# Kernel optimization log

Measured on AMD Instinct MI355X. Metric: run time of the kernel, lower is better.

Reference implementation:

```python
import jax, jax.numpy as jnp
import numpy as np

I_T = 0.5       # IoU threshold self.I_t
GAMMA = 2.0     # focal loss gamma
EPS = 1e-7      # focal loss eps clamp
BS, P, C_IN = 8, 2048, 512


def pairwise_iou(b):
    # b: (bs, P, 4) xyxy -> (bs, P, P), same math as torchvision box_iou (no +1)
    area = (b[..., 2] - b[..., 0]) * (b[..., 3] - b[..., 1])
    lt = jnp.maximum(b[:, :, None, :2], b[:, None, :, :2])
    rb = jnp.minimum(b[:, :, None, 2:], b[:, None, :, 2:])
    wh = jnp.clip(rb - lt, 0.0, None)
    inter = wh[..., 0] * wh[..., 1]
    return inter / (area[:, :, None] + area[:, None, :] - inter)


def assign_labels_weights(pre_score, labels, rois):
    # Vectorized, order-faithful version of the per-batch/per-class python loop.
    # Selected seeds per class c: proposals with pre_score[...,c] > 0.5 if more than
    # one, else the single argmax proposal (torch code falls back when k<=1).
    # Sequential `_I > old` running max over (c, j) in ascending order is equivalent
    # to a global first-occurrence argmax (strict >), so per-class max + running
    # compare with earlier-class tie preference reproduces it exactly.
    bs, Pn = pre_score.shape[0], pre_score.shape[1]
    iou = pairwise_iou(rois)                      # (bs, P, P)
    run_I = jnp.full((bs, Pn), -1.0, pre_score.dtype)
    run_w = jnp.ones((bs, Pn), pre_score.dtype)
    hits = []
    for c in range(3):
        s = pre_score[:, :, c]                    # (bs, P)
        th = s > 0.5
        cnt = th.sum(-1)
        onehot = jnp.arange(Pn)[None, :] == jnp.argmax(s, -1)[:, None]
        sel = jnp.where((cnt > 1)[:, None], th, onehot)
        sel = sel & (labels[:, c] != 0)[:, None]  # skip classes absent from image
        masked = jnp.where(sel[:, None, :], iou, -2.0)  # (bs, P, P)
        val = masked.max(-1)                      # best IoU vs any seed of class c
        jidx = masked.argmax(-1)
        cand_x = jnp.take_along_axis(s, jidx, axis=1)
        better = val > run_I
        run_w = jnp.where(better, cand_x, run_w)
        run_I = jnp.where(better, val, run_I)
        hits.append(val > I_T)
    hit = jnp.stack(hits, -1)                     # (bs, P, 3)
    bg = (~hit.any(-1))[..., None]
    y = jnp.concatenate([hit.astype(pre_score.dtype), bg.astype(pre_score.dtype)], -1)
    return y, run_w


def icr_forward(inputs, fc_w, fc_b, pre_score, labels, rois, num):
    bs = inputs.shape[0] // num
    xr = inputs @ fc_w + fc_b                     # (bs*P, 4)
    logit = jax.nn.softmax(xr.reshape(bs, num, 4), -1)
    ps = jax.lax.stop_gradient(pre_score)         # .clone().detach()
    lb = jax.lax.stop_gradient(labels)
    y, w = assign_labels_weights(ps, lb, rois)
    y = y.reshape(bs * num, 4)
    w = w.reshape(bs * num, 1)
    # FocalLoss(gamma=2, mode='none')
    p = jnp.clip(jax.nn.softmax(xr, -1), EPS, 1.0 - EPS)
    fl = -y * jnp.log(p) * (1.0 - p) ** GAMMA
    imbalance = y.sum(0)                          # (4,)
    loss = (w * fl / (imbalance + 1e-7)).reshape(bs, num, 4)
    lab = lb.at[:, 3].set(1.0)[:, None, :]        # lab[:,0,3]=1
    w_ = 10.0 * jnp.exp(logit) * (1.0 - lab) + lab
    loss = (loss * w_).sum() / bs
    return logit, loss


def setup_inputs():
    key = jax.random.key(0)
    k = jax.random.split(key, 6)
    inputs = jax.random.normal(k[0], (BS * P, C_IN), jnp.float32)
    fc_w = jax.random.normal(k[1], (C_IN, 4), jnp.float32) * 0.02
    fc_b = jnp.zeros((4,), jnp.float32)
    pre_score = jax.random.uniform(k[2], (BS, P, 4), dtype=jnp.float32)
    labels = (jax.random.uniform(k[3], (BS, 4)) < 0.5).astype(jnp.float32)
    labels = labels.at[:, 3].set(0.0)
    xy = jax.random.uniform(k[4], (BS, P, 2), dtype=jnp.float32) * 448.0
    wh = jax.random.uniform(k[5], (BS, P, 2), dtype=jnp.float32) * 63.0 + 1.0
    rois = jnp.concatenate([xy, xy + wh], -1)     # valid xyxy boxes in 512x512
    return {"inputs": inputs, "fc_w": fc_w, "fc_b": fc_b, "pre_score": pre_score,
            "labels": labels, "rois": rois, "num": P}


def reference(inputs, fc_w, fc_b, pre_score, labels, rois, num):
    return icr_forward(inputs, fc_w, fc_b, pre_score, labels, rois, num)
```

## Files before the change

### kernel.cpp

```cpp
#include <hip/hip_runtime.h>

#define BSZ 8
#define PN  2048
#define CIN 512
#define CAP 2048
#define NW  16


__global__ __launch_bounds__(256) void k_front(
    const float* __restrict__ inp, const float* __restrict__ fcw,
    const float* __restrict__ fcb, const float* __restrict__ ps,
    const float* __restrict__ labels, const float* __restrict__ rois,
    float* __restrict__ logit, float* __restrict__ accum,
    int* __restrict__ meta, float* __restrict__ sList,
    float* __restrict__ areaL, float4* __restrict__ roiList)
{
  const int t = threadIdx.x;
  if (blockIdx.x < 1024) {
    const int gw   = (blockIdx.x * 256 + t) >> 6;
    const int lane = t & 63;
    const int kb   = lane << 2;
    const float4 wa0 = *(const float4*)(fcw + (kb + 0) * 4);
    const float4 wa1 = *(const float4*)(fcw + (kb + 1) * 4);
    const float4 wa2 = *(const float4*)(fcw + (kb + 2) * 4);
    const float4 wa3 = *(const float4*)(fcw + (kb + 3) * 4);
    const float4 wb0 = *(const float4*)(fcw + (256 + kb + 0) * 4);
    const float4 wb1 = *(const float4*)(fcw + (256 + kb + 1) * 4);
    const float4 wb2 = *(const float4*)(fcw + (256 + kb + 2) * 4);
    const float4 wb3 = *(const float4*)(fcw + (256 + kb + 3) * 4);
    const float4 bias = *(const float4*)fcb;
    #pragma unroll
    for (int rr = 0; rr < 4; ++rr) {
      const int r = (gw << 2) + rr;
      const float* row = inp + r * CIN;
      const float4 xa = *(const float4*)(row + kb);
      const float4 xb = *(const float4*)(row + 256 + kb);
      float a0 = xa.x*wa0.x + xa.y*wa1.x + xa.z*wa2.x + xa.w*wa3.x
               + xb.x*wb0.x + xb.y*wb1.x + xb.z*wb2.x + xb.w*wb3.x;
      float a1 = xa.x*wa0.y + xa.y*wa1.y + xa.z*wa2.y + xa.w*wa3.y
               + xb.x*wb0.y + xb.y*wb1.y + xb.z*wb2.y + xb.w*wb3.y;
      float a2 = xa.x*wa0.z + xa.y*wa1.z + xa.z*wa2.z + xa.w*wa3.z
               + xb.x*wb0.z + xb.y*wb1.z + xb.z*wb2.z + xb.w*wb3.z;
      float a3 = xa.x*wa0.w + xa.y*wa1.w + xa.z*wa2.w + xa.w*wa3.w
               + xb.x*wb0.w + xb.y*wb1.w + xb.z*wb2.w + xb.w*wb3.w;
      #pragma unroll
      for (int off = 32; off; off >>= 1) {
        a0 += __shfl_xor(a0, off); a1 += __shfl_xor(a1, off);
        a2 += __shfl_xor(a2, off); a3 += __shfl_xor(a3, off);
      }
      if (lane == 0) {
        a0 += bias.x; a1 += bias.y; a2 += bias.z; a3 += bias.w;
        const float m  = fmaxf(fmaxf(a0, a1), fmaxf(a2, a3));
        const float e0 = expf(a0 - m), e1 = expf(a1 - m);
        const float e2 = expf(a2 - m), e3 = expf(a3 - m);
        const float inv = 1.0f / (e0 + e1 + e2 + e3);
        float4 o; o.x = e0*inv; o.y = e1*inv; o.z = e2*inv; o.w = e3*inv;
        *(float4*)(logit + r * 4) = o;
      }
    }
    return;
  }

  const int bc = blockIdx.x - 1024;
  if (bc == 0 && t < 8) accum[t] = 0.0f;
  const int b = bc / 3;
  const int c = bc % 3;
  const int j0 = t * 8;

  float sv[8];
  int   flg = 0, cnt = 0;
  float vmax = -1e30f;
  int   jmax = 0;
  #pragma unroll
  for (int m = 0; m < 8; ++m) {
    const float s = ps[(b * PN + j0 + m) * 4 + c];
    sv[m] = s;
    if (s > 0.5f) { flg |= 1 << m; ++cnt; }
    if (s > vmax) { vmax = s; jmax = j0 + m; }
  }

  __shared__ float lv[256];
  __shared__ int   lj[256];
  __shared__ int   pre[256];
  lv[t] = vmax; lj[t] = jmax; pre[t] = cnt;
  __syncthreads();
  for (int off = 128; off > 0; off >>= 1) {
    if (t < off) {
      const float v2 = lv[t + off]; const int j2 = lj[t + off];
      if (v2 > lv[t] || (v2 == lv[t] && j2 < lj[t])) { lv[t] = v2; lj[t] = j2; }
    }
    __syncthreads();
  }
  for (int off = 1; off < 256; off <<= 1) {
    const int add = (t >= off) ? pre[t - off] : 0;
    __syncthreads();
    pre[t] += add;
    __syncthreads();
  }
  const int  totalTh = pre[255];
  const int  excl    = pre[t] - cnt;
  const int  jArg    = lj[0];
  const bool lab     = labels[b * 4 + c] != 0.0f;
  const int  L    = (!lab) ? 0 : ((totalTh > 1) ? totalTh : 1);
  const int  Lpad = (L + 7) & ~7;

  __shared__ float4 lastRoi;
  __shared__ float  lastS, lastA;
  float4* dstR = roiList + bc * CAP;
  float*  dstS = sList   + bc * CAP;
  float*  dstA = areaL   + bc * CAP;
  const float4* rb = ((const float4*)rois) + b * PN;

  if (lab) {
    if (totalTh > 1) {
      int pos = excl;
      #pragma unroll
      for (int m = 0; m < 8; ++m) {
        if (flg & (1 << m)) {
          const float4 r = rb[j0 + m];
          const float  a = (r.z - r.x) * (r.w - r.y);
          dstR[pos] = r; dstS[pos] = sv[m]; dstA[pos] = a;
          if (pos == L - 1) { lastRoi = r; lastS = sv[m]; lastA = a; }
          ++pos;
        }
      }
    } else if (t == (jArg >> 3)) {
      const float4 r = rb[jArg];
      const float  a = (r.z - r.x) * (r.w - r.y);
      dstR[0] = r; dstS[0] = sv[jArg & 7]; dstA[0] = a;
      lastRoi = r; lastS = sv[jArg & 7]; lastA = a;
    }
  }
  __syncthreads();
  if (t < Lpad - L) { dstR[L + t] = lastRoi; dstS[L + t] = lastS; dstA[L + t] = lastA; }
  if (t == 0) meta[bc] = Lpad;
}

__global__ __launch_bounds__(1024, 8) void k_assign(
    const float* __restrict__ rois, const int* __restrict__ meta,
    const float4* __restrict__ roiList, const float* __restrict__ areaL,
    float* __restrict__ pbn, float* __restrict__ pbd, int* __restrict__ pbp)
{
  const int blk   = blockIdx.x;
  const int h     = blk & 1;
  const int itile = (blk >> 1) & 31;
  const int b     = blk >> 6;
  const int t     = threadIdx.x;
  const int lane  = t & 63;
  const int wv    = t >> 6;

  __shared__ __align__(16) char ldsraw[61440];
  float4* sroi  = (float4*)ldsraw;
  float*  sarea = (float*)(ldsraw + 49152);
  float*  mn    = (float*)ldsraw;
  float*  md    = (float*)(ldsraw + 12288);
  int*    mp    = (int*)(ldsraw + 24576);

  int startc[3], cntc[3];
  #pragma unroll
  for (int c = 0; c < 3; ++c) {
    const int L  = meta[b * 3 + c];
    const int L2 = ((L >> 1) + 7) & ~7;
    const int s0 = h ? L2 : 0;
    const int e0 = h ? L  : L2;
    startc[c] = s0;
    cntc[c]   = e0 - s0;
    if (t < cntc[c]) {
      sroi [c * 1024 + t] = roiList[(b * 3 + c) * CAP + s0 + t];
      sarea[c * 1024 + t] = areaL  [(b * 3 + c) * CAP + s0 + t];
    }
  }
  const int i = (itile << 6) + lane;
  const float4 ri = ((const float4*)rois)[b * PN + i];
  const float areai = (ri.z - ri.x) * (ri.w - ri.y);
  __syncthreads();

  float BN[3], BD[3]; int BP[3];
  #pragma unroll
  for (int c = 0; c < 3; ++c) {
    const int cnt = cntc[c];
    const int C   = (((cnt + 15) >> 4) + 7) & ~7;
    const int g0  = wv * C;
    int g1 = g0 + C; if (g1 > cnt) g1 = cnt;
    float nA = -2.0f, dA = 1.0f, nB = -2.0f, dB = 1.0f;
    int   pA = 0, pB = 0;
    const float4* rbase = sroi  + c * 1024;
    const float*  abase = sarea + c * 1024;

    auto upd = [&](float& n, float& d, int& p,
                   const float4 rj, const float aj, const int pos) {
      const float lx = fmaxf(ri.x, rj.x), ly = fmaxf(ri.y, rj.y);
      const float rx = fminf(ri.z, rj.z), ry = fminf(ri.w, rj.w);
      const float ww = fmaxf(rx - lx, 0.0f), hh = fmaxf(ry - ly, 0.0f);
      const float inter = ww * hh;
      const float uni   = areai + aj - inter;
      if (inter * d > n * uni) { n = inter; d = uni; p = pos; }
    };

    for (int g = g0; g < g1; g += 4) {
      const float4 r0 = rbase[g], r1 = rbase[g+1], r2 = rbase[g+2], r3 = rbase[g+3];
      const float  a0 = abase[g], a1 = abase[g+1], a2 = abase[g+2], a3 = abase[g+3];
      upd(nA, dA, pA, r0, a0, g);
      upd(nB, dB, pB, r2, a2, g + 2);
      upd(nA, dA, pA, r1, a1, g + 1);
      upd(nB, dB, pB, r3, a3, g + 3);
    }
    const float tB = nB * dA, tA = nA * dB;
    if (tB > tA || (tB == tA && pB < pA)) { nA = nB; dA = dB; pA = pB; }
    BN[c] = nA; BD[c] = dA; BP[c] = pA + startc[c];
  }
  __syncthreads();
  #pragma unroll
  for (int c = 0; c < 3; ++c) {
    mn[(c * NW + wv) * 64 + lane] = BN[c];
    md[(c * NW + wv) * 64 + lane] = BD[c];
    mp[(c * NW + wv) * 64 + lane] = BP[c];
  }
  __syncthreads();
  if (wv == 0) {
    #pragma unroll
    for (int c = 0; c < 3; ++c) {
      float bn = BN[c], bd = BD[c]; int bp = BP[c];
      for (int w2 = 1; w2 < NW; ++w2) {
        const float n = mn[(c * NW + w2) * 64 + lane];
        const float d = md[(c * NW + w2) * 64 + lane];
        const int   p = mp[(c * NW + w2) * 64 + lane];
        if (n * bd > bn * d) { bn = n; bd = d; bp = p; }
      }
      const int o = ((b * 3 + c) * 2 + h) * PN + i;
      pbn[o] = bn; pbd[o] = bd; pbp[o] = bp;
    }
  }
}

__global__ __launch_bounds__(256) void k_back(
    const float* __restrict__ pbn, const float* __restrict__ pbd,
    const int* __restrict__ pbp, const float* __restrict__ sList,
    const float* __restrict__ logit, const float* __restrict__ labels,
    float* __restrict__ accum)
{
  const int t  = threadIdx.x;
  const int gi = blockIdx.x * 256 + t;
  const int b  = gi >> 11;
  const int i  = gi & (PN - 1);

  float v[3], sc[3];
  #pragma unroll
  for (int c = 0; c < 3; ++c) {
    const int o0 = ((b * 3 + c) * 2) * PN + i;
    float n = pbn[o0], d = pbd[o0]; int p = pbp[o0];
    const float n1 = pbn[o0 + PN], d1 = pbd[o0 + PN];
    const int   p1 = pbp[o0 + PN];
    if (n1 * d > n * d1) { n = n1; d = d1; p = p1; }
    v[c]  = n / d;
    sc[c] = sList[(b * 3 + c) * CAP + p];
  }
  float runI = -1.0f, runw = 1.0f;
  if (v[0] > runI) { runw = sc[0]; runI = v[0]; }
  if (v[1] > runI) { runw = sc[1]; runI = v[1]; }
  if (v[2] > runI) { runw = sc[2]; runI = v[2]; }
  const float y0 = (v[0] > 0.5f) ? 1.0f : 0.0f;
  const float y1 = (v[1] > 0.5f) ? 1.0f : 0.0f;
  const float y2 = (v[2] > 0.5f) ? 1.0f : 0.0f;
  const float y3 = (y0 + y1 + y2 == 0.0f) ? 1.0f : 0.0f;

  const float4 lg = ((const float4*)logit)[gi];
  const float lb0 = labels[b * 4 + 0];
  const float lb1 = labels[b * 4 + 1];
  const float lb2 = labels[b * 4 + 2];

  auto term = [&](const float l, const float yv, const float labv) -> float {
    const float p  = fminf(fmaxf(l, 1e-7f), 1.0f - 1e-7f);
    const float om = 1.0f - p;
    const float fl = -yv * logf(p) * om * om;
    const float wl = 10.0f * expf(l) * (1.0f - labv) + labv;
    return runw * fl * wl;
  };
  float s[8];
  s[0] = term(lg.x, y0, lb0); s[1] = term(lg.y, y1, lb1);
  s[2] = term(lg.z, y2, lb2); s[3] = term(lg.w, y3, 1.0f);
  s[4] = y0; s[5] = y1; s[6] = y2; s[7] = y3;

  #pragma unroll
  for (int k = 0; k < 8; ++k)
    #pragma unroll
    for (int off = 32; off; off >>= 1) s[k] += __shfl_xor(s[k], off);

  __shared__ float red[4][8];
  const int wv = t >> 6;
  if ((t & 63) == 0)
    #pragma unroll
    for (int k = 0; k < 8; ++k) red[wv][k] = s[k];
  __syncthreads();
  if (t < 8) {
    const float sum = red[0][t] + red[1][t] + red[2][t] + red[3][t];
    atomicAdd(&accum[t], sum);
  }
}

__global__ void k_final(const float* __restrict__ accum, float* __restrict__ loss)
{
  if (threadIdx.x == 0) {
    float L = 0.0f;
    #pragma unroll
    for (int c = 0; c < 4; ++c) L += accum[c] / (accum[4 + c] + 1e-7f);
    loss[0] = L * 0.125f;
  }
}

extern "C" void kernel_launch(void* const* d_in, const int* in_sizes, int n_in,
                              void* d_out, int out_size, void* d_ws, size_t ws_size,
                              hipStream_t stream)
{
  (void)in_sizes; (void)n_in; (void)out_size; (void)ws_size;
  const float* inp    = (const float*)d_in[0];
  const float* fcw    = (const float*)d_in[1];
  const float* fcb    = (const float*)d_in[2];
  const float* ps     = (const float*)d_in[3];
  const float* labels = (const float*)d_in[4];
  const float* rois   = (const float*)d_in[5];
  float* out = (float*)d_out;

  char* ws = (char*)d_ws;
  float*  accum   = (float*) (ws);
  int*    meta    = (int*)   (ws + 64);
  float*  sList   = (float*) (ws + 1024);
  float*  areaL   = (float*) (ws + 197632);
  float4* roiL    = (float4*)(ws + 394240);
  float*  pbn     = (float*) (ws + 1180672);
  float*  pbd     = (float*) (ws + 1573888);
  int*    pbp     = (int*)   (ws + 1967104);

  k_front <<<1048, 256, 0, stream>>>(inp, fcw, fcb, ps, labels, rois,
                                     out, accum, meta, sList, areaL, roiL);
  k_assign<<<512, 1024, 0, stream>>>(rois, meta, roiL, areaL, pbn, pbd, pbp);
  k_back  <<<64,   256, 0, stream>>>(pbn, pbd, pbp, sList, out, labels, accum);
  k_final <<<1,     64, 0, stream>>>(accum, out + BSZ * PN * 4);
}
```

Before: 118.6 us.

## Fuse FC-softmax into IoU assign kernel and fold final reduction into back kernel

Moves the linear+softmax over input rows out of the front kernel and interleaves it with the per-class IoU scans in the assign kernel, staging the weights in LDS. The seed-selection kernel becomes a small standalone launch. The IoU scan now reads seed boxes straight from global memory (uniform per-wave addresses via readfirstlane) instead of staging them in LDS. The final loss kernel is replaced by a last-block ticket in the back kernel, which removes one launch. The intent is to overlap the bandwidth-bound FC with the compute-bound IoU work and cut launch count, at the risk of slower global scalar loads in the IoU loop.

```diff
diff --git a/kernel.cpp b/kernel.cpp
--- a/kernel.cpp
+++ b/kernel.cpp
@@ -7,62 +7,15 @@
 #define NW  16
 
 
-__global__ __launch_bounds__(256) void k_front(
-    const float* __restrict__ inp, const float* __restrict__ fcw,
-    const float* __restrict__ fcb, const float* __restrict__ ps,
-    const float* __restrict__ labels, const float* __restrict__ rois,
-    float* __restrict__ logit, float* __restrict__ accum,
+__global__ __launch_bounds__(256) void k_sel(
+    const float* __restrict__ ps, const float* __restrict__ labels,
+    const float* __restrict__ rois, float* __restrict__ accum,
     int* __restrict__ meta, float* __restrict__ sList,
     float* __restrict__ areaL, float4* __restrict__ roiList)
 {
-  const int t = threadIdx.x;
-  if (blockIdx.x < 1024) {
-    const int gw   = (blockIdx.x * 256 + t) >> 6;
-    const int lane = t & 63;
-    const int kb   = lane << 2;
-    const float4 wa0 = *(const float4*)(fcw + (kb + 0) * 4);
-    const float4 wa1 = *(const float4*)(fcw + (kb + 1) * 4);
-    const float4 wa2 = *(const float4*)(fcw + (kb + 2) * 4);
-    const float4 wa3 = *(const float4*)(fcw + (kb + 3) * 4);
-    const float4 wb0 = *(const float4*)(fcw + (256 + kb + 0) * 4);
-    const float4 wb1 = *(const float4*)(fcw + (256 + kb + 1) * 4);
-    const float4 wb2 = *(const float4*)(fcw + (256 + kb + 2) * 4);
-    const float4 wb3 = *(const float4*)(fcw + (256 + kb + 3) * 4);
-    const float4 bias = *(const float4*)fcb;
-    #pragma unroll
-    for (int rr = 0; rr < 4; ++rr) {
-      const int r = (gw << 2) + rr;
-      const float* row = inp + r * CIN;
-      const float4 xa = *(const float4*)(row + kb);
-      const float4 xb = *(const float4*)(row + 256 + kb);
-      float a0 = xa.x*wa0.x + xa.y*wa1.x + xa.z*wa2.x + xa.w*wa3.x
-               + xb.x*wb0.x + xb.y*wb1.x + xb.z*wb2.x + xb.w*wb3.x;
-      float a1 = xa.x*wa0.y + xa.y*wa1.y + xa.z*wa2.y + xa.w*wa3.y
-               + xb.x*wb0.y + xb.y*wb1.y + xb.z*wb2.y + xb.w*wb3.y;
-      float a2 = xa.x*wa0.z + xa.y*wa1.z + xa.z*wa2.z + xa.w*wa3.z
-               + xb.x*wb0.z + xb.y*wb1.z + xb.z*wb2.z + xb.w*wb3.z;
-      float a3 = xa.x*wa0.w + xa.y*wa1.w + xa.z*wa2.w + xa.w*wa3.w
-               + xb.x*wb0.w + xb.y*wb1.w + xb.z*wb2.w + xb.w*wb3.w;
-      #pragma unroll
-      for (int off = 32; off; off >>= 1) {
-        a0 += __shfl_xor(a0, off); a1 += __shfl_xor(a1, off);
-        a2 += __shfl_xor(a2, off); a3 += __shfl_xor(a3, off);
-      }
-      if (lane == 0) {
-        a0 += bias.x; a1 += bias.y; a2 += bias.z; a3 += bias.w;
-        const float m  = fmaxf(fmaxf(a0, a1), fmaxf(a2, a3));
-        const float e0 = expf(a0 - m), e1 = expf(a1 - m);
-        const float e2 = expf(a2 - m), e3 = expf(a3 - m);
-        const float inv = 1.0f / (e0 + e1 + e2 + e3);
-        float4 o; o.x = e0*inv; o.y = e1*inv; o.z = e2*inv; o.w = e3*inv;
-        *(float4*)(logit + r * 4) = o;
-      }
-    }
-    return;
-  }
-
-  const int bc = blockIdx.x - 1024;
-  if (bc == 0 && t < 8) accum[t] = 0.0f;
+  const int t  = threadIdx.x;
+  const int bc = blockIdx.x;
+  if (bc == 0 && t < 12) accum[t] = 0.0f;
   const int b = bc / 3;
   const int c = bc % 3;
   const int j0 = t * 8;
@@ -136,9 +89,11 @@
   if (t == 0) meta[bc] = Lpad;
 }
 
-__global__ __launch_bounds__(1024, 8) void k_assign(
-    const float* __restrict__ rois, const int* __restrict__ meta,
-    const float4* __restrict__ roiList, const float* __restrict__ areaL,
+__global__ __launch_bounds__(1024, 8) void k_mid(
+    const float* __restrict__ inp, const float* __restrict__ fcw,
+    const float* __restrict__ fcb, const float* __restrict__ rois,
+    const int* __restrict__ meta, const float4* __restrict__ roiList,
+    const float* __restrict__ areaL, float* __restrict__ logit,
     float* __restrict__ pbn, float* __restrict__ pbd, int* __restrict__ pbp)
 {
   const int blk   = blockIdx.x;
@@ -149,67 +104,125 @@
   const int lane  = t & 63;
   const int wv    = t >> 6;
 
-  __shared__ __align__(16) char ldsraw[61440];
-  float4* sroi  = (float4*)ldsraw;
-  float*  sarea = (float*)(ldsraw + 49152);
-  float*  mn    = (float*)ldsraw;
-  float*  md    = (float*)(ldsraw + 12288);
-  int*    mp    = (int*)(ldsraw + 24576);
+  __shared__ float sW[2048];
+  __shared__ float mn[3 * NW * 64];
+  __shared__ float md[3 * NW * 64];
+  __shared__ int   mp[3 * NW * 64];
+
+  const int gw2 = (blk << 4) + wv;
+  const int r0  = gw2 << 1;
+  const int kb  = lane << 2;
+  const float* xrow0 = inp + r0 * CIN;
+  const float4 x0a = *(const float4*)(xrow0 + kb);
+  const float4 x0b = *(const float4*)(xrow0 + 256 + kb);
+  const float4 bias = *(const float4*)fcb;
+
+  {
+    int idx = t;
+    sW[idx] = fcw[(idx & 511) * 4 + (idx >> 9)];
+    idx = t + 1024;
+    sW[idx] = fcw[(idx & 511) * 4 + (idx >> 9)];
+  }
+
+  const int i = (itile << 6) + lane;
+  const float4 ri = ((const float4*)rois)[b * PN + i];
+  const float areai = (ri.z - ri.x) * (ri.w - ri.y);
 
   int startc[3], cntc[3];
   #pragma unroll
   for (int c = 0; c < 3; ++c) {
     const int L  = meta[b * 3 + c];
     const int L2 = ((L >> 1) + 7) & ~7;
-    const int s0 = h ? L2 : 0;
-    const int e0 = h ? L  : L2;
-    startc[c] = s0;
-    cntc[c]   = e0 - s0;
-    if (t < cntc[c]) {
-      sroi [c * 1024 + t] = roiList[(b * 3 + c) * CAP + s0 + t];
-      sarea[c * 1024 + t] = areaL  [(b * 3 + c) * CAP + s0 + t];
-    }
-  }
-  const int i = (itile << 6) + lane;
-  const float4 ri = ((const float4*)rois)[b * PN + i];
-  const float areai = (ri.z - ri.x) * (ri.w - ri.y);
-  __syncthreads();
+    startc[c] = h ? L2 : 0;
+    cntc[c]   = (h ? L : L2) - startc[c];
+  }
 
   float BN[3], BD[3]; int BP[3];
-  #pragma unroll
-  for (int c = 0; c < 3; ++c) {
+
+  auto upd = [&](float& n, float& d, int& p,
+                 const float4 rj, const float aj, const int pos) {
+    const float lx = fmaxf(ri.x, rj.x), ly = fmaxf(ri.y, rj.y);
+    const float rx = fminf(ri.z, rj.z), ry = fminf(ri.w, rj.w);
+    const float ww = fmaxf(rx - lx, 0.0f), hh = fmaxf(ry - ly, 0.0f);
+    const float inter = ww * hh;
+    const float uni   = areai + aj - inter;
+    if (inter * d > n * uni) { n = inter; d = uni; p = pos; }
+  };
+
+  auto iou_c = [&](const int c) {
     const int cnt = cntc[c];
     const int C   = (((cnt + 15) >> 4) + 7) & ~7;
-    const int g0  = wv * C;
+    int g0 = wv * C;
     int g1 = g0 + C; if (g1 > cnt) g1 = cnt;
+    g0 = __builtin_amdgcn_readfirstlane(g0);
+    g1 = __builtin_amdgcn_readfirstlane(g1);
+    const float4* __restrict__ rbase = roiList + (b * 3 + c) * CAP + startc[c];
+    const float*  __restrict__ abase = areaL   + (b * 3 + c) * CAP + startc[c];
     float nA = -2.0f, dA = 1.0f, nB = -2.0f, dB = 1.0f;
     int   pA = 0, pB = 0;
-    const float4* rbase = sroi  + c * 1024;
-    const float*  abase = sarea + c * 1024;
-
-    auto upd = [&](float& n, float& d, int& p,
-                   const float4 rj, const float aj, const int pos) {
-      const float lx = fmaxf(ri.x, rj.x), ly = fmaxf(ri.y, rj.y);
-      const float rx = fminf(ri.z, rj.z), ry = fminf(ri.w, rj.w);
-      const float ww = fmaxf(rx - lx, 0.0f), hh = fmaxf(ry - ly, 0.0f);
-      const float inter = ww * hh;
-      const float uni   = areai + aj - inter;
-      if (inter * d > n * uni) { n = inter; d = uni; p = pos; }
-    };
-
     for (int g = g0; g < g1; g += 4) {
-      const float4 r0 = rbase[g], r1 = rbase[g+1], r2 = rbase[g+2], r3 = rbase[g+3];
-      const float  a0 = abase[g], a1 = abase[g+1], a2 = abase[g+2], a3 = abase[g+3];
-      upd(nA, dA, pA, r0, a0, g);
-      upd(nB, dB, pB, r2, a2, g + 2);
-      upd(nA, dA, pA, r1, a1, g + 1);
-      upd(nB, dB, pB, r3, a3, g + 3);
+      const float4 r0_ = rbase[g],   r1_ = rbase[g+1];
+      const float4 r2_ = rbase[g+2], r3_ = rbase[g+3];
+      const float  a0_ = abase[g],   a1_ = abase[g+1];
+      const float  a2_ = abase[g+2], a3_ = abase[g+3];
+      upd(nA, dA, pA, r0_, a0_, g);
+      upd(nB, dB, pB, r2_, a2_, g + 2);
+      upd(nA, dA, pA, r1_, a1_, g + 1);
+      upd(nB, dB, pB, r3_, a3_, g + 3);
     }
     const float tB = nB * dA, tA = nA * dB;
     if (tB > tA || (tB == tA && pB < pA)) { nA = nB; dA = dB; pA = pB; }
     BN[c] = nA; BD[c] = dA; BP[c] = pA + startc[c];
-  }
-  __syncthreads();
+  };
+
+  auto fc_row = [&](const int r, const float4 xa, const float4 xb) {
+    const float4* w4 = (const float4*)sW;
+    float a0, a1, a2, a3;
+    {
+      const float4 w0 = w4[      lane], w1 = w4[128 + lane];
+      const float4 w2 = w4[256 + lane], w3 = w4[384 + lane];
+      a0 = xa.x*w0.x + xa.y*w0.y + xa.z*w0.z + xa.w*w0.w;
+      a1 = xa.x*w1.x + xa.y*w1.y + xa.z*w1.z + xa.w*w1.w;
+      a2 = xa.x*w2.x + xa.y*w2.y + xa.z*w2.z + xa.w*w2.w;
+      a3 = xa.x*w3.x + xa.y*w3.y + xa.z*w3.z + xa.w*w3.w;
+    }
+    {
+      const float4 w0 = w4[ 64 + lane], w1 = w4[192 + lane];
+      const float4 w2 = w4[320 + lane], w3 = w4[448 + lane];
+      a0 += xb.x*w0.x + xb.y*w0.y + xb.z*w0.z + xb.w*w0.w;
+      a1 += xb.x*w1.x + xb.y*w1.y + xb.z*w1.z + xb.w*w1.w;
+      a2 += xb.x*w2.x + xb.y*w2.y + xb.z*w2.z + xb.w*w2.w;
+      a3 += xb.x*w3.x + xb.y*w3.y + xb.z*w3.z + xb.w*w3.w;
+    }
+    #pragma unroll
+    for (int off = 32; off; off >>= 1) {
+      a0 += __shfl_xor(a0, off); a1 += __shfl_xor(a1, off);
+      a2 += __shfl_xor(a2, off); a3 += __shfl_xor(a3, off);
+    }
+    if (lane == 0) {
+      a0 += bias.x; a1 += bias.y; a2 += bias.z; a3 += bias.w;
+      const float m  = fmaxf(fmaxf(a0, a1), fmaxf(a2, a3));
+      const float e0 = expf(a0 - m), e1 = expf(a1 - m);
+      const float e2 = expf(a2 - m), e3 = expf(a3 - m);
+      const float inv = 1.0f / (e0 + e1 + e2 + e3);
+      float4 o; o.x = e0*inv; o.y = e1*inv; o.z = e2*inv; o.w = e3*inv;
+      *(float4*)(logit + r * 4) = o;
+    }
+  };
+
+  iou_c(0);
+
+  __syncthreads();
+  fc_row(r0, x0a, x0b);
+
+  const float* xrow1 = xrow0 + CIN;
+  const float4 x1a = *(const float4*)(xrow1 + kb);
+  const float4 x1b = *(const float4*)(xrow1 + 256 + kb);
+
+  iou_c(1);
+  fc_row(r0 + 1, x1a, x1b);
+  iou_c(2);
+
   #pragma unroll
   for (int c = 0; c < 3; ++c) {
     mn[(c * NW + wv) * 64 + lane] = BN[c];
@@ -237,7 +250,7 @@
     const float* __restrict__ pbn, const float* __restrict__ pbd,
     const int* __restrict__ pbp, const float* __restrict__ sList,
     const float* __restrict__ logit, const float* __restrict__ labels,
-    float* __restrict__ accum)
+    float* __restrict__ accum, float* __restrict__ loss)
 {
   const int t  = threadIdx.x;
   const int gi = blockIdx.x * 256 + t;
@@ -296,15 +309,23 @@
     const float sum = red[0][t] + red[1][t] + red[2][t] + red[3][t];
     atomicAdd(&accum[t], sum);
   }
-}
-
-__global__ void k_final(const float* __restrict__ accum, float* __restrict__ loss)
-{
-  if (threadIdx.x == 0) {
-    float L = 0.0f;
-    #pragma unroll
-    for (int c = 0; c < 4; ++c) L += accum[c] / (accum[4 + c] + 1e-7f);
-    loss[0] = L * 0.125f;
+  __syncthreads();
+  if (t == 0) {
+    __threadfence();
+    const int ticket = __hip_atomic_fetch_add((int*)(accum + 8), 1,
+                        __ATOMIC_ACQ_REL, __HIP_MEMORY_SCOPE_AGENT);
+    if (ticket == 63) {
+      float L = 0.0f;
+      #pragma unroll
+      for (int c = 0; c < 4; ++c) {
+        const float num = __hip_atomic_load(accum + c,
+                            __ATOMIC_RELAXED, __HIP_MEMORY_SCOPE_AGENT);
+        const float den = __hip_atomic_load(accum + 4 + c,
+                            __ATOMIC_RELAXED, __HIP_MEMORY_SCOPE_AGENT);
+        L += num / (den + 1e-7f);
+      }
+      loss[0] = L * 0.125f;
+    }
   }
 }
 
@@ -331,9 +352,9 @@
   float*  pbd     = (float*) (ws + 1573888);
   int*    pbp     = (int*)   (ws + 1967104);
 
-  k_front <<<1048, 256, 0, stream>>>(inp, fcw, fcb, ps, labels, rois,
-                                     out, accum, meta, sList, areaL, roiL);
-  k_assign<<<512, 1024, 0, stream>>>(rois, meta, roiL, areaL, pbn, pbd, pbp);
-  k_back  <<<64,   256, 0, stream>>>(pbn, pbd, pbp, sList, out, labels, accum);
-  k_final <<<1,     64, 0, stream>>>(accum, out + BSZ * PN * 4);
+  k_sel <<<24,  256,  0, stream>>>(ps, labels, rois, accum, meta, sList, areaL, roiL);
+  k_mid <<<512, 1024, 0, stream>>>(inp, fcw, fcb, rois, meta, roiL, areaL,
+                                   out, pbn, pbd, pbp);
+  k_back<<<64,  256,  0, stream>>>(pbn, pbd, pbp, sList, out, labels, accum,
+                                   out + BSZ * PN * 4);
 }
```

Measured after the change: 121.1 us. +2.1%, slower.

## Move FC softmax into assign kernel, reuse seed loads across two rows, fold final reduction

Applied to the files above, without the earlier changes.

Seed selection now runs alone in a small kernel, and the FC+softmax work moves into the large assign launch as extra blocks, so the GEMV overlaps the IoU argmax. Each assign block now handles two 64-row i tiles per seed load from LDS, halving the block count for the IoU part and reusing shared loads across rows. The final loss kernel is replaced by a last-block ticket atomic inside k_back, which removes one launch. The cost is more registers per thread and extra barriers in the two-pass cross-wave reduction.

```diff
diff --git a/kernel.cpp b/kernel.cpp
--- a/kernel.cpp
+++ b/kernel.cpp
@@ -7,19 +7,104 @@
 #define NW  16
 
 
-__global__ __launch_bounds__(256) void k_front(
-    const float* __restrict__ inp, const float* __restrict__ fcw,
-    const float* __restrict__ fcb, const float* __restrict__ ps,
-    const float* __restrict__ labels, const float* __restrict__ rois,
-    float* __restrict__ logit, float* __restrict__ accum,
+__global__ __launch_bounds__(256) void k_sel(
+    const float* __restrict__ ps, const float* __restrict__ labels,
+    const float* __restrict__ rois, float* __restrict__ accum,
     int* __restrict__ meta, float* __restrict__ sList,
     float* __restrict__ areaL, float4* __restrict__ roiList)
 {
-  const int t = threadIdx.x;
-  if (blockIdx.x < 1024) {
-    const int gw   = (blockIdx.x * 256 + t) >> 6;
-    const int lane = t & 63;
-    const int kb   = lane << 2;
+  const int t  = threadIdx.x;
+  const int bc = blockIdx.x;
+  if (bc == 0 && t < 12) accum[t] = 0.0f;
+  const int b = bc / 3;
+  const int c = bc % 3;
+  const int j0 = t * 8;
+
+  float sv[8];
+  int   flg = 0, cnt = 0;
+  float vmax = -1e30f;
+  int   jmax = 0;
+  #pragma unroll
+  for (int m = 0; m < 8; ++m) {
+    const float s = ps[(b * PN + j0 + m) * 4 + c];
+    sv[m] = s;
+    if (s > 0.5f) { flg |= 1 << m; ++cnt; }
+    if (s > vmax) { vmax = s; jmax = j0 + m; }
+  }
+
+  __shared__ float lv[256];
+  __shared__ int   lj[256];
+  __shared__ int   pre[256];
+  lv[t] = vmax; lj[t] = jmax; pre[t] = cnt;
+  __syncthreads();
+  for (int off = 128; off > 0; off >>= 1) {
+    if (t < off) {
+      const float v2 = lv[t + off]; const int j2 = lj[t + off];
+      if (v2 > lv[t] || (v2 == lv[t] && j2 < lj[t])) { lv[t] = v2; lj[t] = j2; }
+    }
+    __syncthreads();
+  }
+  for (int off = 1; off < 256; off <<= 1) {
+    const int add = (t >= off) ? pre[t - off] : 0;
+    __syncthreads();
+    pre[t] += add;
+    __syncthreads();
+  }
+  const int  totalTh = pre[255];
+  const int  excl    = pre[t] - cnt;
+  const int  jArg    = lj[0];
+  const bool lab     = labels[b * 4 + c] != 0.0f;
+  const int  L    = (!lab) ? 0 : ((totalTh > 1) ? totalTh : 1);
+  const int  Lpad = (L + 7) & ~7;
+
+  __shared__ float4 lastRoi;
+  __shared__ float  lastS, lastA;
+  float4* dstR = roiList + bc * CAP;
+  float*  dstS = sList   + bc * CAP;
+  float*  dstA = areaL   + bc * CAP;
+  const float4* rb = ((const float4*)rois) + b * PN;
+
+  if (lab) {
+    if (totalTh > 1) {
+      int pos = excl;
+      #pragma unroll
+      for (int m = 0; m < 8; ++m) {
+        if (flg & (1 << m)) {
+          const float4 r = rb[j0 + m];
+          const float  a = (r.z - r.x) * (r.w - r.y);
+          dstR[pos] = r; dstS[pos] = sv[m]; dstA[pos] = a;
+          if (pos == L - 1) { lastRoi = r; lastS = sv[m]; lastA = a; }
+          ++pos;
+        }
+      }
+    } else if (t == (jArg >> 3)) {
+      const float4 r = rb[jArg];
+      const float  a = (r.z - r.x) * (r.w - r.y);
+      dstR[0] = r; dstS[0] = sv[jArg & 7]; dstA[0] = a;
+      lastRoi = r; lastS = sv[jArg & 7]; lastA = a;
+    }
+  }
+  __syncthreads();
+  if (t < Lpad - L) { dstR[L + t] = lastRoi; dstS[L + t] = lastS; dstA[L + t] = lastA; }
+  if (t == 0) meta[bc] = Lpad;
+}
+
+__global__ __launch_bounds__(1024, 8) void k_fused(
+    const float* __restrict__ inp, const float* __restrict__ fcw,
+    const float* __restrict__ fcb, const float* __restrict__ rois,
+    const int* __restrict__ meta, const float4* __restrict__ roiList,
+    const float* __restrict__ areaL, float* __restrict__ logit,
+    float* __restrict__ pbn, float* __restrict__ pbd, int* __restrict__ pbp)
+{
+  const int t    = threadIdx.x;
+  const int lane = t & 63;
+  const int wv   = t >> 6;
+
+  __shared__ __align__(16) char ldsraw[61440];
+
+  if (blockIdx.x >= 256) {
+    const int gw = ((int)blockIdx.x - 256) * NW + wv;
+    const int kb = lane << 2;
     const float4 wa0 = *(const float4*)(fcw + (kb + 0) * 4);
     const float4 wa1 = *(const float4*)(fcw + (kb + 1) * 4);
     const float4 wa2 = *(const float4*)(fcw + (kb + 2) * 4);
@@ -61,95 +146,11 @@
     return;
   }
 
-  const int bc = blockIdx.x - 1024;
-  if (bc == 0 && t < 8) accum[t] = 0.0f;
-  const int b = bc / 3;
-  const int c = bc % 3;
-  const int j0 = t * 8;
-
-  float sv[8];
-  int   flg = 0, cnt = 0;
-  float vmax = -1e30f;
-  int   jmax = 0;
-  #pragma unroll
-  for (int m = 0; m < 8; ++m) {
-    const float s = ps[(b * PN + j0 + m) * 4 + c];
-    sv[m] = s;
-    if (s > 0.5f) { flg |= 1 << m; ++cnt; }
-    if (s > vmax) { vmax = s; jmax = j0 + m; }
-  }
-
-  __shared__ float lv[256];
-  __shared__ int   lj[256];
-  __shared__ int   pre[256];
-  lv[t] = vmax; lj[t] = jmax; pre[t] = cnt;
-  __syncthreads();
-  for (int off = 128; off > 0; off >>= 1) {
-    if (t < off) {
-      const float v2 = lv[t + off]; const int j2 = lj[t + off];
-      if (v2 > lv[t] || (v2 == lv[t] && j2 < lj[t])) { lv[t] = v2; lj[t] = j2; }
-    }
-    __syncthreads();
-  }
-  for (int off = 1; off < 256; off <<= 1) {
-    const int add = (t >= off) ? pre[t - off] : 0;
-    __syncthreads();
-    pre[t] += add;
-    __syncthreads();
-  }
-  const int  totalTh = pre[255];
-  const int  excl    = pre[t] - cnt;
-  const int  jArg    = lj[0];
-  const bool lab     = labels[b * 4 + c] != 0.0f;
-  const int  L    = (!lab) ? 0 : ((totalTh > 1) ? totalTh : 1);
-  const int  Lpad = (L + 7) & ~7;
-
-  __shared__ float4 lastRoi;
-  __shared__ float  lastS, lastA;
-  float4* dstR = roiList + bc * CAP;
-  float*  dstS = sList   + bc * CAP;
-  float*  dstA = areaL   + bc * CAP;
-  const float4* rb = ((const float4*)rois) + b * PN;
-
-  if (lab) {
-    if (totalTh > 1) {
-      int pos = excl;
-      #pragma unroll
-      for (int m = 0; m < 8; ++m) {
-        if (flg & (1 << m)) {
-          const float4 r = rb[j0 + m];
-          const float  a = (r.z - r.x) * (r.w - r.y);
-          dstR[pos] = r; dstS[pos] = sv[m]; dstA[pos] = a;
-          if (pos == L - 1) { lastRoi = r; lastS = sv[m]; lastA = a; }
-          ++pos;
-        }
-      }
-    } else if (t == (jArg >> 3)) {
-      const float4 r = rb[jArg];
-      const float  a = (r.z - r.x) * (r.w - r.y);
-      dstR[0] = r; dstS[0] = sv[jArg & 7]; dstA[0] = a;
-      lastRoi = r; lastS = sv[jArg & 7]; lastA = a;
-    }
-  }
-  __syncthreads();
-  if (t < Lpad - L) { dstR[L + t] = lastRoi; dstS[L + t] = lastS; dstA[L + t] = lastA; }
-  if (t == 0) meta[bc] = Lpad;
-}
-
-__global__ __launch_bounds__(1024, 8) void k_assign(
-    const float* __restrict__ rois, const int* __restrict__ meta,
-    const float4* __restrict__ roiList, const float* __restrict__ areaL,
-    float* __restrict__ pbn, float* __restrict__ pbd, int* __restrict__ pbp)
-{
-  const int blk   = blockIdx.x;
-  const int h     = blk & 1;
-  const int itile = (blk >> 1) & 31;
-  const int b     = blk >> 6;
-  const int t     = threadIdx.x;
-  const int lane  = t & 63;
-  const int wv    = t >> 6;
-
-  __shared__ __align__(16) char ldsraw[61440];
+  const int blk = blockIdx.x;
+  const int h   = blk & 1;
+  const int it  = (blk >> 1) & 15;
+  const int b   = blk >> 5;
+
   float4* sroi  = (float4*)ldsraw;
   float*  sarea = (float*)(ldsraw + 49152);
   float*  mn    = (float*)ldsraw;
@@ -170,66 +171,82 @@
       sarea[c * 1024 + t] = areaL  [(b * 3 + c) * CAP + s0 + t];
     }
   }
-  const int i = (itile << 6) + lane;
-  const float4 ri = ((const float4*)rois)[b * PN + i];
-  const float areai = (ri.z - ri.x) * (ri.w - ri.y);
-  __syncthreads();
-
-  float BN[3], BD[3]; int BP[3];
+  const int i0 = (it << 7) + lane;
+  const float4 ri0 = ((const float4*)rois)[b * PN + i0];
+  const float4 ri1 = ((const float4*)rois)[b * PN + i0 + 64];
+  const float ar0 = (ri0.z - ri0.x) * (ri0.w - ri0.y);
+  const float ar1 = (ri1.z - ri1.x) * (ri1.w - ri1.y);
+  __syncthreads();
+
+  auto upd = [](const float4 ri, const float ai,
+                float& n, float& d, int& p,
+                const float4 rj, const float aj, const int pos) {
+    const float lx = fmaxf(ri.x, rj.x), ly = fmaxf(ri.y, rj.y);
+    const float rx = fminf(ri.z, rj.z), ry = fminf(ri.w, rj.w);
+    const float ww = fmaxf(rx - lx, 0.0f), hh = fmaxf(ry - ly, 0.0f);
+    const float inter = ww * hh;
+    const float uni   = ai + aj - inter;
+    if (inter * d > n * uni) { n = inter; d = uni; p = pos; }
+  };
+
+  float BN[3][2], BD[3][2]; int BP[3][2];
   #pragma unroll
   for (int c = 0; c < 3; ++c) {
     const int cnt = cntc[c];
     const int C   = (((cnt + 15) >> 4) + 7) & ~7;
     const int g0  = wv * C;
     int g1 = g0 + C; if (g1 > cnt) g1 = cnt;
-    float nA = -2.0f, dA = 1.0f, nB = -2.0f, dB = 1.0f;
-    int   pA = 0, pB = 0;
     const float4* rbase = sroi  + c * 1024;
     const float*  abase = sarea + c * 1024;
-
-    auto upd = [&](float& n, float& d, int& p,
-                   const float4 rj, const float aj, const int pos) {
-      const float lx = fmaxf(ri.x, rj.x), ly = fmaxf(ri.y, rj.y);
-      const float rx = fminf(ri.z, rj.z), ry = fminf(ri.w, rj.w);
-      const float ww = fmaxf(rx - lx, 0.0f), hh = fmaxf(ry - ly, 0.0f);
-      const float inter = ww * hh;
-      const float uni   = areai + aj - inter;
-      if (inter * d > n * uni) { n = inter; d = uni; p = pos; }
-    };
-
-    for (int g = g0; g < g1; g += 4) {
-      const float4 r0 = rbase[g], r1 = rbase[g+1], r2 = rbase[g+2], r3 = rbase[g+3];
-      const float  a0 = abase[g], a1 = abase[g+1], a2 = abase[g+2], a3 = abase[g+3];
-      upd(nA, dA, pA, r0, a0, g);
-      upd(nB, dB, pB, r2, a2, g + 2);
-      upd(nA, dA, pA, r1, a1, g + 1);
-      upd(nB, dB, pB, r3, a3, g + 3);
-    }
-    const float tB = nB * dA, tA = nA * dB;
-    if (tB > tA || (tB == tA && pB < pA)) { nA = nB; dA = dB; pA = pB; }
-    BN[c] = nA; BD[c] = dA; BP[c] = pA + startc[c];
-  }
-  __syncthreads();
-  #pragma unroll
-  for (int c = 0; c < 3; ++c) {
-    mn[(c * NW + wv) * 64 + lane] = BN[c];
-    md[(c * NW + wv) * 64 + lane] = BD[c];
-    mp[(c * NW + wv) * 64 + lane] = BP[c];
-  }
-  __syncthreads();
-  if (wv == 0) {
+    float n0A = -2.0f, d0A = 1.0f, n0B = -2.0f, d0B = 1.0f;
+    float n1A = -2.0f, d1A = 1.0f, n1B = -2.0f, d1B = 1.0f;
+    int   p0A = 0, p0B = 0, p1A = 0, p1B = 0;
+
+    for (int g = g0; g < g1; g += 2) {
+      const float4 r0_ = rbase[g], r1_ = rbase[g + 1];
+      const float  a0_ = abase[g], a1_ = abase[g + 1];
+      upd(ri0, ar0, n0A, d0A, p0A, r0_, a0_, g);
+      upd(ri1, ar1, n1A, d1A, p1A, r0_, a0_, g);
+      upd(ri0, ar0, n0B, d0B, p0B, r1_, a1_, g + 1);
+      upd(ri1, ar1, n1B, d1B, p1B, r1_, a1_, g + 1);
+    }
+    {
+      const float tB = n0B * d0A, tA = n0A * d0B;
+      if (tB > tA || (tB == tA && p0B < p0A)) { n0A = n0B; d0A = d0B; p0A = p0B; }
+    }
+    {
+      const float tB = n1B * d1A, tA = n1A * d1B;
+      if (tB > tA || (tB == tA && p1B < p1A)) { n1A = n1B; d1A = d1B; p1A = p1B; }
+    }
+    BN[c][0] = n0A; BD[c][0] = d0A; BP[c][0] = p0A + startc[c];
+    BN[c][1] = n1A; BD[c][1] = d1A; BP[c][1] = p1A + startc[c];
+  }
+  __syncthreads();
+  #pragma unroll
+  for (int ii = 0; ii < 2; ++ii) {
     #pragma unroll
     for (int c = 0; c < 3; ++c) {
-      float bn = BN[c], bd = BD[c]; int bp = BP[c];
-      for (int w2 = 1; w2 < NW; ++w2) {
-        const float n = mn[(c * NW + w2) * 64 + lane];
-        const float d = md[(c * NW + w2) * 64 + lane];
-        const int   p = mp[(c * NW + w2) * 64 + lane];
-        if (n * bd > bn * d) { bn = n; bd = d; bp = p; }
-      }
-      const int o = ((b * 3 + c) * 2 + h) * PN + i;
-      pbn[o] = bn; pbd[o] = bd; pbp[o] = bp;
-    }
+      mn[(c * NW + wv) * 64 + lane] = BN[c][ii];
+      md[(c * NW + wv) * 64 + lane] = BD[c][ii];
+      mp[(c * NW + wv) * 64 + lane] = BP[c][ii];
+    }
+    __syncthreads();
+    if (wv == 0) {
+      #pragma unroll
+      for (int c = 0; c < 3; ++c) {
+        float bn = BN[c][ii], bd = BD[c][ii]; int bp = BP[c][ii];
+        for (int w2 = 1; w2 < NW; ++w2) {
+          const float n = mn[(c * NW + w2) * 64 + lane];
+          const float d = md[(c * NW + w2) * 64 + lane];
+          const int   p = mp[(c * NW + w2) * 64 + lane];
+          if (n * bd > bn * d) { bn = n; bd = d; bp = p; }
+        }
+        const int ig = (it << 7) + (ii << 6) + lane;
+        const int o  = ((b * 3 + c) * 2 + h) * PN + ig;
+        pbn[o] = bn; pbd[o] = bd; pbp[o] = bp;
+      }
+    }
+    __syncthreads();
   }
 }
 
@@ -237,7 +254,7 @@
     const float* __restrict__ pbn, const float* __restrict__ pbd,
     const int* __restrict__ pbp, const float* __restrict__ sList,
     const float* __restrict__ logit, const float* __restrict__ labels,
-    float* __restrict__ accum)
+    float* __restrict__ accum, float* __restrict__ loss)
 {
   const int t  = threadIdx.x;
   const int gi = blockIdx.x * 256 + t;
@@ -296,15 +313,23 @@
     const float sum = red[0][t] + red[1][t] + red[2][t] + red[3][t];
     atomicAdd(&accum[t], sum);
   }
-}
-
-__global__ void k_final(const float* __restrict__ accum, float* __restrict__ loss)
-{
-  if (threadIdx.x == 0) {
-    float L = 0.0f;
-    #pragma unroll
-    for (int c = 0; c < 4; ++c) L += accum[c] / (accum[4 + c] + 1e-7f);
-    loss[0] = L * 0.125f;
+  __syncthreads();
+  if (t == 0) {
+    __threadfence();
+    const int ticket = __hip_atomic_fetch_add((int*)(accum + 8), 1,
+                        __ATOMIC_ACQ_REL, __HIP_MEMORY_SCOPE_AGENT);
+    if (ticket == 63) {
+      float L = 0.0f;
+      #pragma unroll
+      for (int c = 0; c < 4; ++c) {
+        const float num = __hip_atomic_load(accum + c,
+                            __ATOMIC_RELAXED, __HIP_MEMORY_SCOPE_AGENT);
+        const float den = __hip_atomic_load(accum + 4 + c,
+                            __ATOMIC_RELAXED, __HIP_MEMORY_SCOPE_AGENT);
+        L += num / (den + 1e-7f);
+      }
+      loss[0] = L * 0.125f;
+    }
   }
 }
 
@@ -331,9 +356,9 @@
   float*  pbd     = (float*) (ws + 1573888);
   int*    pbp     = (int*)   (ws + 1967104);
 
-  k_front <<<1048, 256, 0, stream>>>(inp, fcw, fcb, ps, labels, rois,
-                                     out, accum, meta, sList, areaL, roiL);
-  k_assign<<<512, 1024, 0, stream>>>(rois, meta, roiL, areaL, pbn, pbd, pbp);
-  k_back  <<<64,   256, 0, stream>>>(pbn, pbd, pbp, sList, out, labels, accum);
-  k_final <<<1,     64, 0, stream>>>(accum, out + BSZ * PN * 4);
+  k_sel  <<<24,  256,  0, stream>>>(ps, labels, rois, accum, meta, sList, areaL, roiL);
+  k_fused<<<512, 1024, 0, stream>>>(inp, fcw, fcb, rois, meta, roiL, areaL,
+                                    out, pbn, pbd, pbp);
+  k_back <<<64,  256,  0, stream>>>(pbn, pbd, pbp, sList, out, labels, accum,
+                                    out + BSZ * PN * 4);
 }
```

After: 123.7 us. +4.3%, slower.
